# Performance work log

Measured on AMD Instinct MI355X. Metric: run time of the kernel, lower is better.

## Reference

```python
import jax, jax.numpy as jnp
import numpy as np

N_GRAPHS = 1024   # pool of learnable adjacency blocks (len(Adjs))
BLOCK = 128       # nodes per graph (block size)
BATCH = 1024      # len(batch_idrange); D = BATCH * BLOCK rows
FEAT = 32         # input feature dim


def setup_inputs() -> dict:
    key = jax.random.key(0)
    k1, k2, k3 = jax.random.split(key, 3)
    # learnable per-graph adjacency weights (self.weights stacked)
    weights = jax.random.normal(k1, (N_GRAPHS, BLOCK, BLOCK), dtype=jnp.float32)
    # dense node-feature input [D, F] with D = BATCH * BLOCK
    inp = jax.random.normal(k2, (BATCH * BLOCK, FEAT), dtype=jnp.float32)
    # which adjacency block each batch element uses
    batch_idrange = jax.random.randint(k3, (BATCH,), 0, N_GRAPHS, dtype=jnp.int64)
    return {"input": inp, "weights": weights, "batch_idrange": batch_idrange}


def reference(input, weights, batch_idrange):
    # Original: blockdiag(weights[batch_idrange]) @ input.
    # Block-diagonal structure means each block only touches its own row slab,
    # so this is exactly a batched per-block matmul (same math, no zero padding).
    B = batch_idrange.shape[0]
    n = weights.shape[1]
    W = weights[batch_idrange]                    # [B, n, n] gather (irregular access)
    xb = input.reshape(B, n, -1)                  # [B, n, F]
    out = jnp.einsum('bij,bjf->bif', W, xb)       # [B, n, F]
    return out.reshape(input.shape[0], -1)        # [D, F]
```

## Files before the change

kernel.cpp:

```cpp
#include <hip/hip_runtime.h>

#define NODES 128
#define FEAT  32
#define WPAD  36

__global__ __launch_bounds__(128)
void blockdiag_mm(const float* __restrict__ inp,
                  const float* __restrict__ weights,
                  const int* __restrict__ idx,
                  float* __restrict__ out)
{
    __shared__ __align__(16) float xs[NODES * FEAT];
    __shared__ __align__(16) float ws[NODES * WPAD];

    const int b    = blockIdx.x;
    const int u    = threadIdx.x;
    const int rowg = (u & 7) | ((u >> 6) << 3);
    const int tf   = (u >> 3) & 7;
    const int f0   = tf << 2;

    const float* __restrict__ xin = inp + (size_t)b * (NODES * FEAT);
    const float* __restrict__ wb  = weights + (size_t)idx[b] * (NODES * NODES);

    {
        const float4* src = (const float4*)xin;
        float4* dst = (float4*)xs;
        #pragma unroll
        for (int s = 0; s < 8; ++s)
            dst[s * 128 + u] = src[s * 128 + u];
    }

    float4 acc[8];
    #pragma unroll
    for (int r = 0; r < 8; ++r) acc[r] = make_float4(0.f, 0.f, 0.f, 0.f);

    const int kk = u & 7;
    const int ib = u >> 3;

    for (int c = 0; c < 4; ++c) {
        const int k0 = c * 32;
        #pragma unroll
        for (int s = 0; s < 8; ++s) {
            const int i = ib + (s << 4);
            const float4 v = *(const float4*)(wb + i * NODES + k0 + (kk << 2));
            *(float4*)(ws + i * WPAD + (kk << 2)) = v;
        }
        __syncthreads();

        #pragma unroll
        for (int kc = 0; kc < 8; ++kc) {
            const float4 bv0 = *(const float4*)(xs + (k0 + kc * 4 + 0) * FEAT + f0);
            const float4 bv1 = *(const float4*)(xs + (k0 + kc * 4 + 1) * FEAT + f0);
            const float4 bv2 = *(const float4*)(xs + (k0 + kc * 4 + 2) * FEAT + f0);
            const float4 bv3 = *(const float4*)(xs + (k0 + kc * 4 + 3) * FEAT + f0);
            #pragma unroll
            for (int r = 0; r < 8; ++r) {
                const float4 av = *(const float4*)(ws + (rowg + 16 * r) * WPAD + (kc << 2));
                acc[r].x += av.x * bv0.x; acc[r].y += av.x * bv0.y; acc[r].z += av.x * bv0.z; acc[r].w += av.x * bv0.w;
                acc[r].x += av.y * bv1.x; acc[r].y += av.y * bv1.y; acc[r].z += av.y * bv1.z; acc[r].w += av.y * bv1.w;
                acc[r].x += av.z * bv2.x; acc[r].y += av.z * bv2.y; acc[r].z += av.z * bv2.z; acc[r].w += av.z * bv2.w;
                acc[r].x += av.w * bv3.x; acc[r].y += av.w * bv3.y; acc[r].z += av.w * bv3.z; acc[r].w += av.w * bv3.w;
            }
        }
        __syncthreads();
    }

    float* ob = out + (size_t)b * (NODES * FEAT);
    #pragma unroll
    for (int r = 0; r < 8; ++r)
        *(float4*)(ob + (rowg + 16 * r) * FEAT + f0) = acc[r];
}

extern "C" void kernel_launch(void* const* d_in, const int* in_sizes, int n_in,
                              void* d_out, int out_size, void* d_ws, size_t ws_size,
                              hipStream_t stream) {
    const float* inp = (const float*)d_in[0];
    const float* wts = (const float*)d_in[1];
    const int*   idx = (const int*)d_in[2];
    float* outp = (float*)d_out;
    const int B = in_sizes[2];
    hipLaunchKernelGGL(blockdiag_mm, dim3(B), dim3(128), 0, stream,
                       inp, wts, idx, outp);
}
```

Before: 121.8 us.

## Double-buffer weight tiles via direct global-to-LDS loads with 256 threads

Stages the input and weight tiles into shared memory with direct global-to-LDS load instructions, so values no longer pass through registers. Weights are split into smaller 16-wide k-chunks and double-buffered, so the next chunk loads while the current one is computed. An XOR swizzle replaces the row padding to avoid bank conflicts. The block grows to 256 threads with fewer accumulators each, which aims at better latency hiding and occupancy, at the cost of more barriers and reliance on correct wait semantics for the asynchronous LDS loads.

```diff
diff --git a/kernel.cpp b/kernel.cpp
--- a/kernel.cpp
+++ b/kernel.cpp
@@ -2,60 +2,74 @@
 
 #define NODES 128
 #define FEAT  32
-#define WPAD  36
+#define CK    16
+#define NCH   (NODES / CK)
 
-__global__ __launch_bounds__(128)
+typedef const __attribute__((address_space(1))) void gvoid;
+typedef __attribute__((address_space(3))) void       svoid;
+
+__global__ __launch_bounds__(256, 4)
 void blockdiag_mm(const float* __restrict__ inp,
                   const float* __restrict__ weights,
                   const int* __restrict__ idx,
                   float* __restrict__ out)
 {
     __shared__ __align__(16) float xs[NODES * FEAT];
-    __shared__ __align__(16) float ws[NODES * WPAD];
+    __shared__ __align__(16) float ws[2][NODES * CK];
 
     const int b    = blockIdx.x;
     const int u    = threadIdx.x;
-    const int rowg = (u & 7) | ((u >> 6) << 3);
-    const int tf   = (u >> 3) & 7;
-    const int f0   = tf << 2;
+    const int w    = u >> 6;
+    const int f0   = (u & 7) << 2;
+    const int rowb = u >> 3;
+    const int swz  = rowb & 3;
 
     const float* __restrict__ xin = inp + (size_t)b * (NODES * FEAT);
     const float* __restrict__ wb  = weights + (size_t)idx[b] * (NODES * NODES);
 
-    {
-        const float4* src = (const float4*)xin;
-        float4* dst = (float4*)xs;
-        #pragma unroll
-        for (int s = 0; s < 8; ++s)
-            dst[s * 128 + u] = src[s * 128 + u];
+    #pragma unroll
+    for (int s = 0; s < 4; ++s) {
+        gvoid* g = (gvoid*)(xin + (s * 256 + u) * 4);
+        svoid* l = (svoid*)(xs + (s * 256 + w * 64) * 4);
+        __builtin_amdgcn_global_load_lds(g, l, 16, 0, 0);
     }
 
-    float4 acc[8];
+    auto stage_w = [&](int c, int p) {
+        #pragma unroll
+        for (int s = 0; s < 2; ++s) {
+            const int d4  = s * 256 + u;
+            const int row = d4 >> 2;
+            const int c4  = d4 & 3;
+            const int k4  = c4 ^ (row & 3);
+            gvoid* g = (gvoid*)(wb + row * NODES + c * CK + (k4 << 2));
+            svoid* l = (svoid*)(&ws[p][0] + (s * 256 + w * 64) * 4);
+            __builtin_amdgcn_global_load_lds(g, l, 16, 0, 0);
+        }
+    };
+
+    stage_w(0, 0);
+
+    float4 acc[4];
     #pragma unroll
-    for (int r = 0; r < 8; ++r) acc[r] = make_float4(0.f, 0.f, 0.f, 0.f);
+    for (int r = 0; r < 4; ++r) acc[r] = make_float4(0.f, 0.f, 0.f, 0.f);
 
-    const int kk = u & 7;
-    const int ib = u >> 3;
+    __syncthreads();
 
-    for (int c = 0; c < 4; ++c) {
-        const int k0 = c * 32;
-        #pragma unroll
-        for (int s = 0; s < 8; ++s) {
-            const int i = ib + (s << 4);
-            const float4 v = *(const float4*)(wb + i * NODES + k0 + (kk << 2));
-            *(float4*)(ws + i * WPAD + (kk << 2)) = v;
-        }
-        __syncthreads();
+    for (int c = 0; c < NCH; ++c) {
+        if (c + 1 < NCH) stage_w(c + 1, (c + 1) & 1);
+        const float* __restrict__ wsp = &ws[c & 1][0];
 
         #pragma unroll
-        for (int kc = 0; kc < 8; ++kc) {
-            const float4 bv0 = *(const float4*)(xs + (k0 + kc * 4 + 0) * FEAT + f0);
-            const float4 bv1 = *(const float4*)(xs + (k0 + kc * 4 + 1) * FEAT + f0);
-            const float4 bv2 = *(const float4*)(xs + (k0 + kc * 4 + 2) * FEAT + f0);
-            const float4 bv3 = *(const float4*)(xs + (k0 + kc * 4 + 3) * FEAT + f0);
+        for (int kc = 0; kc < 4; ++kc) {
+            const int kb = c * CK + kc * 4;
+            const float4 bv0 = *(const float4*)(xs + (kb + 0) * FEAT + f0);
+            const float4 bv1 = *(const float4*)(xs + (kb + 1) * FEAT + f0);
+            const float4 bv2 = *(const float4*)(xs + (kb + 2) * FEAT + f0);
+            const float4 bv3 = *(const float4*)(xs + (kb + 3) * FEAT + f0);
+            const int cidx = (kc ^ swz) << 2;
             #pragma unroll
-            for (int r = 0; r < 8; ++r) {
-                const float4 av = *(const float4*)(ws + (rowg + 16 * r) * WPAD + (kc << 2));
+            for (int r = 0; r < 4; ++r) {
+                const float4 av = *(const float4*)(wsp + (rowb + 32 * r) * CK + cidx);
                 acc[r].x += av.x * bv0.x; acc[r].y += av.x * bv0.y; acc[r].z += av.x * bv0.z; acc[r].w += av.x * bv0.w;
                 acc[r].x += av.y * bv1.x; acc[r].y += av.y * bv1.y; acc[r].z += av.y * bv1.z; acc[r].w += av.y * bv1.w;
                 acc[r].x += av.z * bv2.x; acc[r].y += av.z * bv2.y; acc[r].z += av.z * bv2.z; acc[r].w += av.z * bv2.w;
@@ -67,8 +81,8 @@
 
     float* ob = out + (size_t)b * (NODES * FEAT);
     #pragma unroll
-    for (int r = 0; r < 8; ++r)
-        *(float4*)(ob + (rowg + 16 * r) * FEAT + f0) = acc[r];
+    for (int r = 0; r < 4; ++r)
+        *(float4*)(ob + (rowb + 32 * r) * FEAT + f0) = acc[r];
 }
 
 extern "C" void kernel_launch(void* const* d_in, const int* in_sizes, int n_in,
@@ -79,6 +93,6 @@
     const int*   idx = (const int*)d_in[2];
     float* outp = (float*)d_out;
     const int B = in_sizes[2];
-    hipLaunchKernelGGL(blockdiag_mm, dim3(B), dim3(128), 0, stream,
+    hipLaunchKernelGGL(blockdiag_mm, dim3(B), dim3(256), 0, stream,
                        inp, wts, idx, outp);
 }
```

After: 118.8 us. 1.03x faster.

## Use bf16 MFMA with register-prefetched weights instead of fp32 FMA tiles

Applied to the files above, without the earlier changes.

Replaces the scalar fp32 FMA inner loop with 16x16x32 bf16 MFMA instructions. Weights are loaded directly from global memory into registers, with the next k-chunk prefetched, and converted to bf16 in-register rather than staged through shared memory. The input is transposed into a padded bf16 shared tile. The block grows to 256 threads (4 waves), and the per-chunk shared-memory syncs are removed. This lowers compute and LDS traffic but reduces precision to bf16 operands, which risks accuracy tolerance.

```diff
diff --git a/kernel.cpp b/kernel.cpp
--- a/kernel.cpp
+++ b/kernel.cpp
@@ -2,73 +2,113 @@
 
 #define NODES 128
 #define FEAT  32
-#define WPAD  36
+#define XPAD  136
 
-__global__ __launch_bounds__(128)
+typedef __attribute__((ext_vector_type(8))) short bf16x8;
+typedef __attribute__((ext_vector_type(4))) float f32x4;
+
+__device__ __forceinline__ unsigned pk_bf16(float a, float b) {
+    unsigned ua = __builtin_bit_cast(unsigned, a);
+    unsigned ub = __builtin_bit_cast(unsigned, b);
+    ua += 0x7fffu + ((ua >> 16) & 1u);
+    ub += 0x7fffu + ((ub >> 16) & 1u);
+    return (ua >> 16) | (ub & 0xffff0000u);
+}
+
+__device__ __forceinline__ bf16x8 cvt_frag(float4 lo, float4 hi) {
+    union { unsigned u[4]; bf16x8 v; } r;
+    r.u[0] = pk_bf16(lo.x, lo.y);
+    r.u[1] = pk_bf16(lo.z, lo.w);
+    r.u[2] = pk_bf16(hi.x, hi.y);
+    r.u[3] = pk_bf16(hi.z, hi.w);
+    return r.v;
+}
+
+__global__ __launch_bounds__(256, 4)
 void blockdiag_mm(const float* __restrict__ inp,
                   const float* __restrict__ weights,
                   const int* __restrict__ idx,
                   float* __restrict__ out)
 {
-    __shared__ __align__(16) float xs[NODES * FEAT];
-    __shared__ __align__(16) float ws[NODES * WPAD];
+    __shared__ __align__(16) short xt[FEAT * XPAD];
 
-    const int b    = blockIdx.x;
-    const int u    = threadIdx.x;
-    const int rowg = (u & 7) | ((u >> 6) << 3);
-    const int tf   = (u >> 3) & 7;
-    const int f0   = tf << 2;
+    const int b  = blockIdx.x;
+    const int u  = threadIdx.x;
+    const int w  = u >> 6;
+    const int l  = u & 63;
+    const int ln = l & 15;
+    const int q  = l >> 4;
 
     const float* __restrict__ xin = inp + (size_t)b * (NODES * FEAT);
     const float* __restrict__ wb  = weights + (size_t)idx[b] * (NODES * NODES);
 
-    {
-        const float4* src = (const float4*)xin;
-        float4* dst = (float4*)xs;
-        #pragma unroll
-        for (int s = 0; s < 8; ++s)
-            dst[s * 128 + u] = src[s * 128 + u];
+    float4 a_cur[2][2], a_nxt[2][2];
+    #pragma unroll
+    for (int mt = 0; mt < 2; ++mt) {
+        const float* r = wb + (32 * w + 16 * mt + ln) * NODES + q * 8;
+        a_cur[mt][0] = *(const float4*)(r);
+        a_cur[mt][1] = *(const float4*)(r + 4);
     }
 
-    float4 acc[8];
+    {
+        const float4* x4 = (const float4*)xin;
+        const int fq = u & 7;
+        const int kh = (u >> 3) & 31;
+        #pragma unroll
+        for (int rr = 0; rr < 2; ++rr) {
+            const int k0 = rr * 64 + kh * 2;
+            float4 v0 = x4[k0 * 8 + fq];
+            float4 v1 = x4[(k0 + 1) * 8 + fq];
+            const float pv0[4] = {v0.x, v0.y, v0.z, v0.w};
+            const float pv1[4] = {v1.x, v1.y, v1.z, v1.w};
+            #pragma unroll
+            for (int i = 0; i < 4; ++i)
+                *(unsigned*)(&xt[(fq * 4 + i) * XPAD + k0]) = pk_bf16(pv0[i], pv1[i]);
+        }
+    }
+    __syncthreads();
+
+    f32x4 acc[2][2] = {};
+
     #pragma unroll
-    for (int r = 0; r < 8; ++r) acc[r] = make_float4(0.f, 0.f, 0.f, 0.f);
-
-    const int kk = u & 7;
-    const int ib = u >> 3;
-
-    for (int c = 0; c < 4; ++c) {
-        const int k0 = c * 32;
-        #pragma unroll
-        for (int s = 0; s < 8; ++s) {
-            const int i = ib + (s << 4);
-            const float4 v = *(const float4*)(wb + i * NODES + k0 + (kk << 2));
-            *(float4*)(ws + i * WPAD + (kk << 2)) = v;
-        }
-        __syncthreads();
-
-        #pragma unroll
-        for (int kc = 0; kc < 8; ++kc) {
-            const float4 bv0 = *(const float4*)(xs + (k0 + kc * 4 + 0) * FEAT + f0);
-            const float4 bv1 = *(const float4*)(xs + (k0 + kc * 4 + 1) * FEAT + f0);
-            const float4 bv2 = *(const float4*)(xs + (k0 + kc * 4 + 2) * FEAT + f0);
-            const float4 bv3 = *(const float4*)(xs + (k0 + kc * 4 + 3) * FEAT + f0);
+    for (int kc = 0; kc < 4; ++kc) {
+        if (kc < 3) {
             #pragma unroll
-            for (int r = 0; r < 8; ++r) {
-                const float4 av = *(const float4*)(ws + (rowg + 16 * r) * WPAD + (kc << 2));
-                acc[r].x += av.x * bv0.x; acc[r].y += av.x * bv0.y; acc[r].z += av.x * bv0.z; acc[r].w += av.x * bv0.w;
-                acc[r].x += av.y * bv1.x; acc[r].y += av.y * bv1.y; acc[r].z += av.y * bv1.z; acc[r].w += av.y * bv1.w;
-                acc[r].x += av.z * bv2.x; acc[r].y += av.z * bv2.y; acc[r].z += av.z * bv2.z; acc[r].w += av.z * bv2.w;
-                acc[r].x += av.w * bv3.x; acc[r].y += av.w * bv3.y; acc[r].z += av.w * bv3.z; acc[r].w += av.w * bv3.w;
+            for (int mt = 0; mt < 2; ++mt) {
+                const float* r = wb + (32 * w + 16 * mt + ln) * NODES + (kc + 1) * 32 + q * 8;
+                a_nxt[mt][0] = *(const float4*)(r);
+                a_nxt[mt][1] = *(const float4*)(r + 4);
             }
         }
-        __syncthreads();
+        bf16x8 bfr[2];
+        #pragma unroll
+        for (int nt = 0; nt < 2; ++nt)
+            bfr[nt] = *(const bf16x8*)(&xt[(16 * nt + ln) * XPAD + kc * 32 + q * 8]);
+        bf16x8 afr[2];
+        #pragma unroll
+        for (int mt = 0; mt < 2; ++mt)
+            afr[mt] = cvt_frag(a_cur[mt][0], a_cur[mt][1]);
+        #pragma unroll
+        for (int mt = 0; mt < 2; ++mt)
+            #pragma unroll
+            for (int nt = 0; nt < 2; ++nt)
+                acc[mt][nt] = __builtin_amdgcn_mfma_f32_16x16x32_bf16(
+                    afr[mt], bfr[nt], acc[mt][nt], 0, 0, 0);
+        #pragma unroll
+        for (int mt = 0; mt < 2; ++mt) {
+            a_cur[mt][0] = a_nxt[mt][0];
+            a_cur[mt][1] = a_nxt[mt][1];
+        }
     }
 
     float* ob = out + (size_t)b * (NODES * FEAT);
     #pragma unroll
-    for (int r = 0; r < 8; ++r)
-        *(float4*)(ob + (rowg + 16 * r) * FEAT + f0) = acc[r];
+    for (int mt = 0; mt < 2; ++mt)
+        #pragma unroll
+        for (int nt = 0; nt < 2; ++nt)
+            #pragma unroll
+            for (int reg = 0; reg < 4; ++reg)
+                ob[(32 * w + 16 * mt + q * 4 + reg) * FEAT + 16 * nt + ln] = acc[mt][nt][reg];
 }
 
 extern "C" void kernel_launch(void* const* d_in, const int* in_sizes, int n_in,
@@ -79,6 +119,6 @@
     const int*   idx = (const int*)d_in[2];
     float* outp = (float*)d_out;
     const int B = in_sizes[2];
-    hipLaunchKernelGGL(blockdiag_mm, dim3(B), dim3(128), 0, stream,
+    hipLaunchKernelGGL(blockdiag_mm, dim3(B), dim3(256), 0, stream,
                        inp, wts, idx, outp);
 }
```

Measured after the change: 112.2 us. 7.8% less time.
